# Kernel tuning notes

Measured on AMD Instinct MI355X. Metric: run time of the kernel, lower is better.

The kernel has to match this reference:

```python
import jax, jax.numpy as jnp
import numpy as np

B, S, H = 2, 1024, 2048          # batch, seq, hidden
E, K = 8, 2                       # num experts, top-k
I = 1408                          # moe_intermediate_size
IS = 5632                         # shared_expert_intermediate_size
WSCALE = 0.02


def setup_inputs() -> dict:
    key = jax.random.key(0)
    ks = jax.random.split(key, 9)
    f32 = jnp.float32
    return {
        "hidden_states": jax.random.normal(ks[0], (B, S, H), dtype=f32),
        "gate_w": jax.random.normal(ks[1], (E, H), dtype=f32) * WSCALE,          # router
        "w_gate": jax.random.normal(ks[2], (E, H, I), dtype=f32) * WSCALE,       # experts.N.gate_proj
        "w_up": jax.random.normal(ks[3], (E, H, I), dtype=f32) * WSCALE,         # experts.N.up_proj
        "w_down": jax.random.normal(ks[4], (E, I, H), dtype=f32) * WSCALE,       # experts.N.down_proj
        "sw_gate": jax.random.normal(ks[5], (H, IS), dtype=f32) * WSCALE,        # shared_expert.gate_proj
        "sw_up": jax.random.normal(ks[6], (H, IS), dtype=f32) * WSCALE,          # shared_expert.up_proj
        "sw_down": jax.random.normal(ks[7], (IS, H), dtype=f32) * WSCALE,        # shared_expert.down_proj
        "shared_gate_w": jax.random.normal(ks[8], (H, 1), dtype=f32) * WSCALE,   # shared_expert_gate
    }


def reference(hidden_states, gate_w, w_gate, w_up, w_down, sw_gate, sw_up, sw_down, shared_gate_w):
    x = hidden_states                                   # [B,S,H]
    # ---- TopKGate: softmax router -> top-k weights + indices, renormalized ----
    logits = jnp.einsum("bsh,eh->bse", x, gate_w)       # [B,S,E]
    probs = jax.nn.softmax(logits, axis=-1)
    top_w, top_i = jax.lax.top_k(probs, K)              # [B,S,K]
    top_w = top_w / jnp.sum(top_w, axis=-1, keepdims=True)
    # dense combine weights per expert: sum_k top_w * (top_i == e)  -> [B,S,E]
    onehot = jax.nn.one_hot(top_i, E, dtype=x.dtype)    # [B,S,K,E]
    combine = jnp.einsum("bsk,bske->bse", top_w, onehot)
    # ---- dense all-experts SwiGLU MLP, then mask/combine (faithful to source) ----
    g = jnp.einsum("bsh,ehi->besi", x, w_gate)          # [B,E,S,I]
    u = jnp.einsum("bsh,ehi->besi", x, w_up)
    h = jax.nn.silu(g) * u
    expert_out = jnp.einsum("besi,eih->besh", h, w_down)  # [B,E,S,H]
    moe_out = jnp.einsum("besh,bse->bsh", expert_out, combine)
    # ---- shared expert with sigmoid gate ----
    sh = jax.nn.silu(x @ sw_gate) * (x @ sw_up)         # [B,S,IS]
    shared_out = sh @ sw_down                            # [B,S,H]
    shared_gate = jax.nn.sigmoid(x @ shared_gate_w)     # [B,S,1]
    return moe_out + shared_out * shared_gate
```

## Files before the change

### kernel.cpp

```cpp
#include <hip/hip_runtime.h>
#include <hip/hip_bf16.h>
#include <stdint.h>

#define TOK   2048
#define HDIM  2048
#define IDIM  1408
#define ISDIM 5632
#define NEXP  8

typedef float  f32x4  __attribute__((ext_vector_type(4)));
typedef short  bf16x8 __attribute__((ext_vector_type(8)));

__device__ __forceinline__ unsigned short f2b(float f) {
  union { float f; uint32_t u; } v; v.f = f;
  return (unsigned short)((v.u + 0x7fffu + ((v.u >> 16) & 1u)) >> 16);
}

__global__ __launch_bounds__(256) void router_kernel(
    const float* __restrict__ X, const float* __restrict__ GW,
    const float* __restrict__ SGW, int* __restrict__ cnt,
    int* __restrict__ tok_e, float* __restrict__ tok_w, float* __restrict__ sg)
{
  const int tkn = blockIdx.x, t = threadIdx.x;
  const float* xr = X + (size_t)tkn * HDIM;
  float a[NEXP + 1];
  #pragma unroll
  for (int e = 0; e <= NEXP; ++e) a[e] = 0.f;
  for (int h = t; h < HDIM; h += 256) {
    const float xv = xr[h];
    #pragma unroll
    for (int e = 0; e < NEXP; ++e) a[e] += xv * GW[e * HDIM + h];
    a[NEXP] += xv * SGW[h];
  }
  #pragma unroll
  for (int off = 32; off > 0; off >>= 1) {
    #pragma unroll
    for (int e = 0; e <= NEXP; ++e) a[e] += __shfl_down(a[e], off);
  }
  __shared__ float red[4][NEXP + 1];
  if ((t & 63) == 0) {
    #pragma unroll
    for (int e = 0; e <= NEXP; ++e) red[t >> 6][e] = a[e];
  }
  __syncthreads();
  if (t == 0) {
    float l[NEXP + 1];
    #pragma unroll
    for (int e = 0; e <= NEXP; ++e) l[e] = red[0][e] + red[1][e] + red[2][e] + red[3][e];
    int i1 = 0;
    #pragma unroll
    for (int e = 1; e < NEXP; ++e) if (l[e] > l[i1]) i1 = e;
    int i2 = (i1 == 0) ? 1 : 0;
    #pragma unroll
    for (int e = 0; e < NEXP; ++e) if (e != i1 && e != i2 && l[e] > l[i2]) i2 = e;
    const float w1 = 1.f / (1.f + __expf(l[i2] - l[i1]));
    tok_e[tkn * 2 + 0] = i1; tok_e[tkn * 2 + 1] = i2;
    tok_w[tkn * 2 + 0] = w1; tok_w[tkn * 2 + 1] = 1.f - w1;
    atomicAdd(&cnt[i1], 1); atomicAdd(&cnt[i2], 1);
    sg[tkn] = 1.f / (1.f + __expf(-l[NEXP]));
  }
}

__global__ void scan_kernel(const int* __restrict__ cnt, int* __restrict__ offs) {
  if (threadIdx.x == 0) {
    int r = 0;
    for (int e = 0; e < NEXP; ++e) { offs[e] = r; r += cnt[e]; }
  }
}

__global__ __launch_bounds__(256) void build_kernel(
    const int* __restrict__ tok_e, const float* __restrict__ tok_w,
    const int* __restrict__ offs, int* __restrict__ cur,
    int* __restrict__ list, float* __restrict__ wl)
{
  const int tkn = blockIdx.x * 256 + threadIdx.x;
  if (tkn >= TOK) return;
  #pragma unroll
  for (int k = 0; k < 2; ++k) {
    const int e = tok_e[tkn * 2 + k];
    const int pos = atomicAdd(&cur[e], 1);
    const int slot = offs[e] + pos;
    list[slot] = tkn;
    wl[slot] = tok_w[tkn * 2 + k];
  }
}

__global__ __launch_bounds__(256) void cvt_kernel(
    const float* __restrict__ src, unsigned short* __restrict__ dst, int n4)
{
  const int i = blockIdx.x * 512 + threadIdx.x;
  #pragma unroll
  for (int p = 0; p < 2; ++p) {
    const int j = i + p * 256;
    if (j < n4) {
      const float4 v = ((const float4*)src)[j];
      ushort4 b; b.x = f2b(v.x); b.y = f2b(v.y); b.z = f2b(v.z); b.w = f2b(v.w);
      ((ushort4*)dst)[j] = b;
    }
  }
}

__global__ __launch_bounds__(256) void transpose_cvt_kernel(
    const float* __restrict__ src, unsigned short* __restrict__ dst,
    const int R, const int C)
{
  __shared__ unsigned short tile[64][72];
  const size_t mat = (size_t)blockIdx.z * R * C;
  const int c0 = blockIdx.x * 64, r0 = blockIdx.y * 64;
  const int t = threadIdx.x;
  const int rr = t >> 4, cc = (t & 15) * 4;
  #pragma unroll
  for (int p = 0; p < 4; ++p) {
    const int r = rr + p * 16;
    const float4 v = *(const float4*)(src + mat + (size_t)(r0 + r) * C + c0 + cc);
    tile[cc + 0][r] = f2b(v.x);
    tile[cc + 1][r] = f2b(v.y);
    tile[cc + 2][r] = f2b(v.z);
    tile[cc + 3][r] = f2b(v.w);
  }
  __syncthreads();
  #pragma unroll
  for (int p = 0; p < 2; ++p) {
    const int id = p * 256 + t;
    const int c = id >> 3, q = id & 7;
    const uint4 v = *(const uint4*)&tile[c][q * 8];
    *(uint4*)(dst + mat + (size_t)(c0 + c) * R + r0 + q * 8) = v;
  }
}


template<bool GATHER>
__global__ __launch_bounds__(256) void gateup_bf_kernel(
    const unsigned short* __restrict__ Xb,
    const unsigned short* __restrict__ WgT,
    const unsigned short* __restrict__ WuT,
    unsigned short* __restrict__ Cout,
    const int* __restrict__ list, const int* __restrict__ offs,
    const int* __restrict__ cnt, const int N)
{
  __shared__ char smem[49152];
  char* sA  = smem;
  char* sBg = smem + 16384;
  char* sBu = smem + 32768;

  const int t = threadIdx.x;
  const int nt = blockIdx.x;
  int rowbase, mcnt;
  const unsigned short *Wg, *Wu;
  if (GATHER) {
    const int e  = blockIdx.y >> 4;
    const int mt = blockIdx.y & 15;
    mcnt = cnt[e] - mt * 128;
    if (mcnt <= 0) return;
    rowbase = offs[e] + mt * 128;
    Wg = WgT + (size_t)e * N * HDIM;
    Wu = WuT + (size_t)e * N * HDIM;
  } else {
    rowbase = blockIdx.y * 128;
    mcnt = 128;
    Wg = WgT; Wu = WuT;
  }
  const int n0 = nt * 128;

  const int w = t >> 6, lane = t & 63;
  const int wr = w >> 1, wc = w & 1;
  const int lcol = lane & 15, lk = lane >> 4;

  f32x4 accg[4][4], accu[4][4];
  #pragma unroll
  for (int i = 0; i < 4; ++i)
    #pragma unroll
    for (int j = 0; j < 4; ++j) { accg[i][j] = {0.f,0.f,0.f,0.f}; accu[i][j] = {0.f,0.f,0.f,0.f}; }

  int arow[4], bm[4], koff[4];
  #pragma unroll
  for (int p = 0; p < 4; ++p) {
    const int s = p * 256 + t;
    const int m = s >> 3;
    bm[p] = m;
    koff[p] = ((s & 7) ^ (m & 7)) << 3;
    arow[p] = GATHER ? list[rowbase + m] : (rowbase + m);
  }

  const int KSTEPS = HDIM / 64;
  for (int kt = 0; kt < KSTEPS; ++kt) {
    const int k0 = kt * 64;
    if (kt) __syncthreads();
    #pragma unroll
    for (int p = 0; p < 4; ++p) {
      const int s16 = (p * 256 + t) * 16;
      *(uint4*)(sA  + s16) = *(const uint4*)(Xb + (size_t)arow[p] * HDIM + k0 + koff[p]);
      *(uint4*)(sBg + s16) = *(const uint4*)(Wg + (size_t)(n0 + bm[p]) * HDIM + k0 + koff[p]);
      *(uint4*)(sBu + s16) = *(const uint4*)(Wu + (size_t)(n0 + bm[p]) * HDIM + k0 + koff[p]);
    }
    __syncthreads();
    #pragma unroll
    for (int ks = 0; ks < 2; ++ks) {
      bf16x8 af[4], bg[4], bu[4];
      #pragma unroll
      for (int fm = 0; fm < 4; ++fm) {
        const int m = wr * 64 + fm * 16 + lcol;
        af[fm] = *(const bf16x8*)(sA + m * 128 + (((ks * 4 + lk) ^ (m & 7)) << 4));
      }
      #pragma unroll
      for (int fn = 0; fn < 4; ++fn) {
        const int n = wc * 64 + fn * 16 + lcol;
        const int ra = n * 128 + (((ks * 4 + lk) ^ (n & 7)) << 4);
        bg[fn] = *(const bf16x8*)(sBg + ra);
        bu[fn] = *(const bf16x8*)(sBu + ra);
      }
      #pragma unroll
      for (int fm = 0; fm < 4; ++fm)
        #pragma unroll
        for (int fn = 0; fn < 4; ++fn) {
          accg[fm][fn] = __builtin_amdgcn_mfma_f32_16x16x32_bf16(af[fm], bg[fn], accg[fm][fn], 0, 0, 0);
          accu[fm][fn] = __builtin_amdgcn_mfma_f32_16x16x32_bf16(af[fm], bu[fn], accu[fm][fn], 0, 0, 0);
        }
    }
  }
  #pragma unroll
  for (int fm = 0; fm < 4; ++fm) {
    #pragma unroll
    for (int fn = 0; fn < 4; ++fn) {
      const int col = n0 + wc * 64 + fn * 16 + lcol;
      #pragma unroll
      for (int r = 0; r < 4; ++r) {
        const int lrow = wr * 64 + fm * 16 + lk * 4 + r;
        if (lrow < mcnt) {
          const float gv = accg[fm][fn][r];
          const float uv = accu[fm][fn][r];
          const float hv = gv * uv / (1.f + __expf(-gv));
          Cout[(size_t)(rowbase + lrow) * N + col] = f2b(hv);
        }
      }
    }
  }
}

template<bool EXPERT>
__global__ __launch_bounds__(256) void down_bf_kernel(
    const unsigned short* __restrict__ Abuf,
    const unsigned short* __restrict__ BT,
    float* __restrict__ out,
    const int* __restrict__ list, const float* __restrict__ wl,
    const int* __restrict__ offs, const int* __restrict__ cnt, const int K)
{
  __shared__ char smem[32768];
  char* sA = smem;
  char* sB = smem + 16384;

  const int t = threadIdx.x;
  const int nt = blockIdx.x;
  int rowbase, mcnt;
  const unsigned short* Bm;
  if (EXPERT) {
    const int e  = blockIdx.y >> 4;
    const int mt = blockIdx.y & 15;
    mcnt = cnt[e] - mt * 128;
    if (mcnt <= 0) return;
    rowbase = offs[e] + mt * 128;
    Bm = BT + (size_t)e * HDIM * K;
  } else {
    rowbase = blockIdx.y * 128;
    mcnt = 128;
    Bm = BT;
  }
  const int n0 = nt * 128;
  const int w = t >> 6, lane = t & 63;
  const int wr = w >> 1, wc = w & 1;
  const int lcol = lane & 15, lk = lane >> 4;

  f32x4 acc[4][4];
  #pragma unroll
  for (int i = 0; i < 4; ++i)
    #pragma unroll
    for (int j = 0; j < 4; ++j) acc[i][j] = {0.f,0.f,0.f,0.f};

  int bm[4], koff[4];
  #pragma unroll
  for (int p = 0; p < 4; ++p) {
    const int s = p * 256 + t;
    const int m = s >> 3;
    bm[p] = m;
    koff[p] = ((s & 7) ^ (m & 7)) << 3;
  }

  const int KSTEPS = K / 64;
  for (int kt = 0; kt < KSTEPS; ++kt) {
    const int k0 = kt * 64;
    if (kt) __syncthreads();
    #pragma unroll
    for (int p = 0; p < 4; ++p) {
      const int s16 = (p * 256 + t) * 16;
      *(uint4*)(sA + s16) = *(const uint4*)(Abuf + (size_t)(rowbase + bm[p]) * K + k0 + koff[p]);
      *(uint4*)(sB + s16) = *(const uint4*)(Bm + (size_t)(n0 + bm[p]) * K + k0 + koff[p]);
    }
    __syncthreads();
    #pragma unroll
    for (int ks = 0; ks < 2; ++ks) {
      bf16x8 af[4], bfr[4];
      #pragma unroll
      for (int fm = 0; fm < 4; ++fm) {
        const int m = wr * 64 + fm * 16 + lcol;
        af[fm] = *(const bf16x8*)(sA + m * 128 + (((ks * 4 + lk) ^ (m & 7)) << 4));
      }
      #pragma unroll
      for (int fn = 0; fn < 4; ++fn) {
        const int n = wc * 64 + fn * 16 + lcol;
        bfr[fn] = *(const bf16x8*)(sB + n * 128 + (((ks * 4 + lk) ^ (n & 7)) << 4));
      }
      #pragma unroll
      for (int fm = 0; fm < 4; ++fm)
        #pragma unroll
        for (int fn = 0; fn < 4; ++fn)
          acc[fm][fn] = __builtin_amdgcn_mfma_f32_16x16x32_bf16(af[fm], bfr[fn], acc[fm][fn], 0, 0, 0);
    }
  }
  #pragma unroll
  for (int fm = 0; fm < 4; ++fm) {
    #pragma unroll
    for (int fn = 0; fn < 4; ++fn) {
      const int col = n0 + wc * 64 + fn * 16 + lcol;
      #pragma unroll
      for (int r = 0; r < 4; ++r) {
        const int lrow = wr * 64 + fm * 16 + lk * 4 + r;
        if (lrow < mcnt) {
          const float v = acc[fm][fn][r];
          if (EXPERT) {
            const int slot = rowbase + lrow;
            atomicAdd(out + (size_t)list[slot] * HDIM + col, wl[slot] * v);
          } else {
            const int row = rowbase + lrow;
            out[(size_t)row * HDIM + col] = wl[row] * v;
          }
        }
      }
    }
  }
}

template<bool GATHER>
__global__ __launch_bounds__(256) void gateup_kernel(
    const float* __restrict__ X,
    const float* __restrict__ WgA, const float* __restrict__ WuA,
    unsigned short* __restrict__ Cout,
    const int* __restrict__ list, const int* __restrict__ offs,
    const int* __restrict__ cnt, const int N)
{
  __shared__ char smem[49152];
  char* sA  = smem;
  char* sBg = smem + 16384;
  char* sBu = smem + 32768;
  const int t = threadIdx.x;
  const int nt = blockIdx.x;
  int rowbase, mcnt;
  const float *Wg, *Wu;
  if (GATHER) {
    const int e  = blockIdx.y >> 4;
    const int mt = blockIdx.y & 15;
    mcnt = cnt[e] - mt * 128;
    if (mcnt <= 0) return;
    rowbase = offs[e] + mt * 128;
    Wg = WgA + (size_t)e * HDIM * N;
    Wu = WuA + (size_t)e * HDIM * N;
  } else {
    rowbase = blockIdx.y * 128;
    mcnt = 128;
    Wg = WgA; Wu = WuA;
  }
  const int n0 = nt * 128;
  const int w = t >> 6, lane = t & 63;
  const int wr = w >> 1, wc = w & 1;
  const int lcol = lane & 15, lk = lane >> 4;
  f32x4 accg[4][4], accu[4][4];
  #pragma unroll
  for (int i = 0; i < 4; ++i)
    #pragma unroll
    for (int j = 0; j < 4; ++j) { accg[i][j] = {0.f,0.f,0.f,0.f}; accu[i][j] = {0.f,0.f,0.f,0.f}; }
  int arow[8];
  #pragma unroll
  for (int p = 0; p < 8; ++p) {
    const int m = p * 16 + (t >> 4);
    arow[p] = GATHER ? list[rowbase + m] : (rowbase + m);
  }
  const int ak4 = (t & 15) << 2;
  const int bn = t & 127, bkh = t >> 7;
  const int KSTEPS = HDIM / 64;
  for (int kt = 0; kt < KSTEPS; ++kt) {
    const int k0 = kt * 64;
    if (kt) __syncthreads();
    #pragma unroll
    for (int p = 0; p < 8; ++p) {
      const int m = p * 16 + (t >> 4);
      const float4 v = *(const float4*)(X + (size_t)arow[p] * HDIM + k0 + ak4);
      ushort4 b; b.x = f2b(v.x); b.y = f2b(v.y); b.z = f2b(v.z); b.w = f2b(v.w);
      *(ushort4*)(sA + m * 128 + ((((ak4 >> 3) ^ (m & 7)) << 4) | ((ak4 & 7) << 1))) = b;
    }
    #pragma unroll
    for (int p = 0; p < 8; ++p) {
      const int k4 = (p << 1) | bkh;
      const size_t gb = (size_t)(k0 + (k4 << 2)) * N + n0 + bn;
      const int wa = bn * 128 + ((((k4 >> 1) ^ (bn & 7)) << 4) | ((k4 & 1) << 3));
      ushort4 vg, vu;
      vg.x = f2b(Wg[gb]);                 vu.x = f2b(Wu[gb]);
      vg.y = f2b(Wg[gb + (size_t)N]);     vu.y = f2b(Wu[gb + (size_t)N]);
      vg.z = f2b(Wg[gb + 2*(size_t)N]);   vu.z = f2b(Wu[gb + 2*(size_t)N]);
      vg.w = f2b(Wg[gb + 3*(size_t)N]);   vu.w = f2b(Wu[gb + 3*(size_t)N]);
      *(ushort4*)(sBg + wa) = vg;
      *(ushort4*)(sBu + wa) = vu;
    }
    __syncthreads();
    #pragma unroll
    for (int ks = 0; ks < 2; ++ks) {
      bf16x8 af[4], bg[4], bu[4];
      #pragma unroll
      for (int fm = 0; fm < 4; ++fm) {
        const int m = wr * 64 + fm * 16 + lcol;
        af[fm] = *(const bf16x8*)(sA + m * 128 + (((ks * 4 + lk) ^ (m & 7)) << 4));
      }
      #pragma unroll
      for (int fn = 0; fn < 4; ++fn) {
        const int n = wc * 64 + fn * 16 + lcol;
        const int ra = n * 128 + (((ks * 4 + lk) ^ (n & 7)) << 4);
        bg[fn] = *(const bf16x8*)(sBg + ra);
        bu[fn] = *(const bf16x8*)(sBu + ra);
      }
      #pragma unroll
      for (int fm = 0; fm < 4; ++fm)
        #pragma unroll
        for (int fn = 0; fn < 4; ++fn) {
          accg[fm][fn] = __builtin_amdgcn_mfma_f32_16x16x32_bf16(af[fm], bg[fn], accg[fm][fn], 0, 0, 0);
          accu[fm][fn] = __builtin_amdgcn_mfma_f32_16x16x32_bf16(af[fm], bu[fn], accu[fm][fn], 0, 0, 0);
        }
    }
  }
  #pragma unroll
  for (int fm = 0; fm < 4; ++fm) {
    #pragma unroll
    for (int fn = 0; fn < 4; ++fn) {
      const int col = n0 + wc * 64 + fn * 16 + lcol;
      #pragma unroll
      for (int r = 0; r < 4; ++r) {
        const int lrow = wr * 64 + fm * 16 + lk * 4 + r;
        if (lrow < mcnt) {
          const float gv = accg[fm][fn][r];
          const float uv = accu[fm][fn][r];
          Cout[(size_t)(rowbase + lrow) * N + col] = f2b(gv * uv / (1.f + __expf(-gv)));
        }
      }
    }
  }
}

template<bool EXPERT>
__global__ __launch_bounds__(256) void down_kernel(
    const unsigned short* __restrict__ Abuf,
    const float* __restrict__ Ball,
    float* __restrict__ out,
    const int* __restrict__ list, const float* __restrict__ wl,
    const int* __restrict__ offs, const int* __restrict__ cnt, const int K)
{
  __shared__ char smem[32768];
  char* sA = smem;
  char* sB = smem + 16384;
  const int t = threadIdx.x;
  const int nt = blockIdx.x;
  int rowbase, mcnt;
  const float* Bm;
  if (EXPERT) {
    const int e  = blockIdx.y >> 4;
    const int mt = blockIdx.y & 15;
    mcnt = cnt[e] - mt * 128;
    if (mcnt <= 0) return;
    rowbase = offs[e] + mt * 128;
    Bm = Ball + (size_t)e * K * HDIM;
  } else {
    rowbase = blockIdx.y * 128;
    mcnt = 128;
    Bm = Ball;
  }
  const int n0 = nt * 128;
  const int w = t >> 6, lane = t & 63;
  const int wr = w >> 1, wc = w & 1;
  const int lcol = lane & 15, lk = lane >> 4;
  f32x4 acc[4][4];
  #pragma unroll
  for (int i = 0; i < 4; ++i)
    #pragma unroll
    for (int j = 0; j < 4; ++j) acc[i][j] = {0.f,0.f,0.f,0.f};
  const int bn = t & 127, bkh = t >> 7;
  const int KSTEPS = K / 64;
  for (int kt = 0; kt < KSTEPS; ++kt) {
    const int k0 = kt * 64;
    if (kt) __syncthreads();
    #pragma unroll
    for (int p = 0; p < 4; ++p) {
      const int s = p * 256 + t;
      const int m = s >> 3;
      const int k8 = (s & 7) ^ (m & 7);
      const uint4 v = *(const uint4*)(Abuf + (size_t)(rowbase + m) * K + k0 + (k8 << 3));
      *(uint4*)(sA + s * 16) = v;
    }
    #pragma unroll
    for (int p = 0; p < 8; ++p) {
      const int k4 = (p << 1) | bkh;
      const size_t gb = (size_t)(k0 + (k4 << 2)) * HDIM + n0 + bn;
      const int wa = bn * 128 + ((((k4 >> 1) ^ (bn & 7)) << 4) | ((k4 & 1) << 3));
      ushort4 vb;
      vb.x = f2b(Bm[gb]);
      vb.y = f2b(Bm[gb + HDIM]);
      vb.z = f2b(Bm[gb + 2 * HDIM]);
      vb.w = f2b(Bm[gb + 3 * HDIM]);
      *(ushort4*)(sB + wa) = vb;
    }
    __syncthreads();
    #pragma unroll
    for (int ks = 0; ks < 2; ++ks) {
      bf16x8 af[4], bfr[4];
      #pragma unroll
      for (int fm = 0; fm < 4; ++fm) {
        const int m = wr * 64 + fm * 16 + lcol;
        af[fm] = *(const bf16x8*)(sA + m * 128 + (((ks * 4 + lk) ^ (m & 7)) << 4));
      }
      #pragma unroll
      for (int fn = 0; fn < 4; ++fn) {
        const int n = wc * 64 + fn * 16 + lcol;
        bfr[fn] = *(const bf16x8*)(sB + n * 128 + (((ks * 4 + lk) ^ (n & 7)) << 4));
      }
      #pragma unroll
      for (int fm = 0; fm < 4; ++fm)
        #pragma unroll
        for (int fn = 0; fn < 4; ++fn)
          acc[fm][fn] = __builtin_amdgcn_mfma_f32_16x16x32_bf16(af[fm], bfr[fn], acc[fm][fn], 0, 0, 0);
    }
  }
  #pragma unroll
  for (int fm = 0; fm < 4; ++fm) {
    #pragma unroll
    for (int fn = 0; fn < 4; ++fn) {
      const int col = n0 + wc * 64 + fn * 16 + lcol;
      #pragma unroll
      for (int r = 0; r < 4; ++r) {
        const int lrow = wr * 64 + fm * 16 + lk * 4 + r;
        if (lrow < mcnt) {
          const float v = acc[fm][fn][r];
          if (EXPERT) {
            const int slot = rowbase + lrow;
            atomicAdd(out + (size_t)list[slot] * HDIM + col, wl[slot] * v);
          } else {
            const int row = rowbase + lrow;
            out[(size_t)row * HDIM + col] = wl[row] * v;
          }
        }
      }
    }
  }
}

extern "C" void kernel_launch(void* const* d_in, const int* in_sizes, int n_in,
                              void* d_out, int out_size, void* d_ws, size_t ws_size,
                              hipStream_t stream)
{
  const float* x       = (const float*)d_in[0];
  const float* gate_w  = (const float*)d_in[1];
  const float* w_gate  = (const float*)d_in[2];
  const float* w_up    = (const float*)d_in[3];
  const float* w_down  = (const float*)d_in[4];
  const float* sw_gate = (const float*)d_in[5];
  const float* sw_up   = (const float*)d_in[6];
  const float* sw_down = (const float*)d_in[7];
  const float* sgw     = (const float*)d_in[8];

  float* out = (float*)d_out;
  char* ws = (char*)d_ws;

  const size_t NEED = 136000000;

  if (ws_size >= NEED) {
    unsigned short* Xb   = (unsigned short*)ws;
    unsigned short* R1a  = (unsigned short*)(ws + 8388608);
    unsigned short* R1b  = (unsigned short*)(ws + 54525952);
    unsigned short* shb  = (unsigned short*)(ws + 100663296);
    unsigned short* hb   = (unsigned short*)(ws + 123731968);
    char* meta = ws + 135626752;
    int*   cnt   = (int*)(meta);
    int*   cur   = (int*)(meta + 256);
    int*   offs  = (int*)(meta + 512);
    int*   list  = (int*)(meta + 768);
    float* wl    = (float*)(meta + 768 + 17152);
    int*   tok_e = (int*)(meta + 768 + 2 * 17152);
    float* tok_w = (float*)(meta + 768 + 2 * 17152 + 16384);
    float* sg    = (float*)(meta + 768 + 2 * 17152 + 32768);

    hipMemsetAsync(meta, 0, 768 + 2 * 17152, stream);

    cvt_kernel<<<TOK * HDIM / 4 / 512, 256, 0, stream>>>(x, Xb, TOK * HDIM / 4);
    router_kernel<<<TOK, 256, 0, stream>>>(x, gate_w, sgw, cnt, tok_e, tok_w, sg);
    scan_kernel<<<1, 64, 0, stream>>>(cnt, offs);
    build_kernel<<<8, 256, 0, stream>>>(tok_e, tok_w, offs, cur, list, wl);

    transpose_cvt_kernel<<<dim3(ISDIM / 64, HDIM / 64, 1), 256, 0, stream>>>(sw_gate, R1a, HDIM, ISDIM);
    transpose_cvt_kernel<<<dim3(ISDIM / 64, HDIM / 64, 1), 256, 0, stream>>>(sw_up,   R1b, HDIM, ISDIM);
    gateup_bf_kernel<false><<<dim3(ISDIM / 128, TOK / 128), 256, 0, stream>>>(
        Xb, R1a, R1b, shb, nullptr, nullptr, nullptr, ISDIM);
    transpose_cvt_kernel<<<dim3(HDIM / 64, ISDIM / 64, 1), 256, 0, stream>>>(sw_down, R1a, ISDIM, HDIM);
    down_bf_kernel<false><<<dim3(HDIM / 128, TOK / 128), 256, 0, stream>>>(
        shb, R1a, out, nullptr, sg, nullptr, nullptr, ISDIM);
    transpose_cvt_kernel<<<dim3(IDIM / 64, HDIM / 64, NEXP), 256, 0, stream>>>(w_gate, R1a, HDIM, IDIM);
    transpose_cvt_kernel<<<dim3(IDIM / 64, HDIM / 64, NEXP), 256, 0, stream>>>(w_up,   R1b, HDIM, IDIM);
    gateup_bf_kernel<true><<<dim3(IDIM / 128, NEXP * 16), 256, 0, stream>>>(
        Xb, R1a, R1b, hb, list, offs, cnt, IDIM);
    transpose_cvt_kernel<<<dim3(HDIM / 64, IDIM / 64, NEXP), 256, 0, stream>>>(w_down, R1a, IDIM, HDIM);
    down_bf_kernel<true><<<dim3(HDIM / 128, NEXP * 16), 256, 0, stream>>>(
        hb, R1a, out, list, wl, offs, cnt, IDIM);
  } else {
    unsigned short* sh_buf = (unsigned short*)ws;
    unsigned short* h_buf  = (unsigned short*)(ws + 23068672);
    char* meta = ws + 34963456;
    int*   cnt   = (int*)(meta);
    int*   cur   = (int*)(meta + 256);
    int*   offs  = (int*)(meta + 512);
    int*   list  = (int*)(meta + 768);
    float* wl    = (float*)(meta + 768 + 17152);
    int*   tok_e = (int*)(meta + 768 + 2 * 17152);
    float* tok_w = (float*)(meta + 768 + 2 * 17152 + 16384);
    float* sg    = (float*)(meta + 768 + 2 * 17152 + 32768);

    hipMemsetAsync(meta, 0, 768 + 2 * 17152, stream);
    router_kernel<<<TOK, 256, 0, stream>>>(x, gate_w, sgw, cnt, tok_e, tok_w, sg);
    scan_kernel<<<1, 64, 0, stream>>>(cnt, offs);
    build_kernel<<<8, 256, 0, stream>>>(tok_e, tok_w, offs, cur, list, wl);
    gateup_kernel<false><<<dim3(ISDIM / 128, TOK / 128), 256, 0, stream>>>(
        x, sw_gate, sw_up, sh_buf, nullptr, nullptr, nullptr, ISDIM);
    down_kernel<false><<<dim3(HDIM / 128, TOK / 128), 256, 0, stream>>>(
        sh_buf, sw_down, out, nullptr, sg, nullptr, nullptr, ISDIM);
    gateup_kernel<true><<<dim3(IDIM / 128, NEXP * 16), 256, 0, stream>>>(
        x, w_gate, w_up, h_buf, list, offs, cnt, IDIM);
    down_kernel<true><<<dim3(HDIM / 128, NEXP * 16), 256, 0, stream>>>(
        h_buf, w_down, out, list, wl, offs, cnt, IDIM);
  }
}
```

Before: 645.4 us.

## Use direct global-to-LDS loads, XCD-aware block swizzle, and split-K shared down-proj

```diff
diff --git a/kernel.cpp b/kernel.cpp
--- a/kernel.cpp
+++ b/kernel.cpp
@@ -14,6 +14,12 @@
 __device__ __forceinline__ unsigned short f2b(float f) {
   union { float f; uint32_t u; } v; v.f = f;
   return (unsigned short)((v.u + 0x7fffu + ((v.u >> 16) & 1u)) >> 16);
+}
+
+__device__ __forceinline__ void async16(void* lds, const void* g) {
+  __builtin_amdgcn_global_load_lds(
+      (const __attribute__((address_space(1))) unsigned int*)g,
+      (__attribute__((address_space(3))) unsigned int*)lds, 16, 0, 0);
 }
 
 __global__ __launch_bounds__(256) void router_kernel(
@@ -136,31 +142,35 @@
     const unsigned short* __restrict__ WuT,
     unsigned short* __restrict__ Cout,
     const int* __restrict__ list, const int* __restrict__ offs,
-    const int* __restrict__ cnt, const int N)
+    const int* __restrict__ cnt, const int N, const int NT)
 {
   __shared__ char smem[49152];
   char* sA  = smem;
   char* sBg = smem + 16384;
   char* sBu = smem + 32768;
 
+  int wg = blockIdx.x;
+  wg = (wg & 7) * (gridDim.x >> 3) + (wg >> 3);
+  const int mt = wg & 15;
+  const int pn = wg >> 4;
+
   const int t = threadIdx.x;
-  const int nt = blockIdx.x;
-  int rowbase, mcnt;
+  int rowbase, mcnt, n0;
   const unsigned short *Wg, *Wu;
   if (GATHER) {
-    const int e  = blockIdx.y >> 4;
-    const int mt = blockIdx.y & 15;
+    const int e = pn / NT, n = pn % NT;
     mcnt = cnt[e] - mt * 128;
     if (mcnt <= 0) return;
     rowbase = offs[e] + mt * 128;
+    n0 = n * 128;
     Wg = WgT + (size_t)e * N * HDIM;
     Wu = WuT + (size_t)e * N * HDIM;
   } else {
-    rowbase = blockIdx.y * 128;
+    rowbase = mt * 128;
     mcnt = 128;
+    n0 = pn * 128;
     Wg = WgT; Wu = WuT;
   }
-  const int n0 = nt * 128;
 
   const int w = t >> 6, lane = t & 63;
   const int wr = w >> 1, wc = w & 1;
@@ -188,10 +198,10 @@
     if (kt) __syncthreads();
     #pragma unroll
     for (int p = 0; p < 4; ++p) {
-      const int s16 = (p * 256 + t) * 16;
-      *(uint4*)(sA  + s16) = *(const uint4*)(Xb + (size_t)arow[p] * HDIM + k0 + koff[p]);
-      *(uint4*)(sBg + s16) = *(const uint4*)(Wg + (size_t)(n0 + bm[p]) * HDIM + k0 + koff[p]);
-      *(uint4*)(sBu + s16) = *(const uint4*)(Wu + (size_t)(n0 + bm[p]) * HDIM + k0 + koff[p]);
+      const int lb = (p * 256 + (t & 192)) * 16;
+      async16(sA  + lb, Xb + (size_t)arow[p] * HDIM + k0 + koff[p]);
+      async16(sBg + lb, Wg + (size_t)(n0 + bm[p]) * HDIM + k0 + koff[p]);
+      async16(sBu + lb, Wu + (size_t)(n0 + bm[p]) * HDIM + k0 + koff[p]);
     }
     __syncthreads();
     #pragma unroll
@@ -237,35 +247,41 @@
   }
 }
 
-template<bool EXPERT>
+template<bool EXPERT, int KSPLIT>
 __global__ __launch_bounds__(256) void down_bf_kernel(
     const unsigned short* __restrict__ Abuf,
     const unsigned short* __restrict__ BT,
     float* __restrict__ out,
     const int* __restrict__ list, const float* __restrict__ wl,
-    const int* __restrict__ offs, const int* __restrict__ cnt, const int K)
+    const int* __restrict__ offs, const int* __restrict__ cnt,
+    const int K, const int ktps)
 {
   __shared__ char smem[32768];
   char* sA = smem;
   char* sB = smem + 16384;
 
+  int wg = blockIdx.x;
+  wg = (wg & 7) * (gridDim.x >> 3) + (wg >> 3);
+  const int ksp = wg % KSPLIT;
+  const int mt  = (wg / KSPLIT) & 15;
+  const int pn  = wg / (KSPLIT * 16);
+
   const int t = threadIdx.x;
-  const int nt = blockIdx.x;
-  int rowbase, mcnt;
+  int rowbase, mcnt, n0;
   const unsigned short* Bm;
   if (EXPERT) {
-    const int e  = blockIdx.y >> 4;
-    const int mt = blockIdx.y & 15;
+    const int e = pn >> 4, n = pn & 15;
     mcnt = cnt[e] - mt * 128;
     if (mcnt <= 0) return;
     rowbase = offs[e] + mt * 128;
+    n0 = n * 128;
     Bm = BT + (size_t)e * HDIM * K;
   } else {
-    rowbase = blockIdx.y * 128;
+    rowbase = mt * 128;
     mcnt = 128;
+    n0 = pn * 128;
     Bm = BT;
   }
-  const int n0 = nt * 128;
   const int w = t >> 6, lane = t & 63;
   const int wr = w >> 1, wc = w & 1;
   const int lcol = lane & 15, lk = lane >> 4;
@@ -285,15 +301,15 @@
     koff[p] = ((s & 7) ^ (m & 7)) << 3;
   }
 
-  const int KSTEPS = K / 64;
-  for (int kt = 0; kt < KSTEPS; ++kt) {
+  const int kbeg = ksp * ktps, kend = kbeg + ktps;
+  for (int kt = kbeg; kt < kend; ++kt) {
     const int k0 = kt * 64;
-    if (kt) __syncthreads();
+    if (kt != kbeg) __syncthreads();
     #pragma unroll
     for (int p = 0; p < 4; ++p) {
-      const int s16 = (p * 256 + t) * 16;
-      *(uint4*)(sA + s16) = *(const uint4*)(Abuf + (size_t)(rowbase + bm[p]) * K + k0 + koff[p]);
-      *(uint4*)(sB + s16) = *(const uint4*)(Bm + (size_t)(n0 + bm[p]) * K + k0 + koff[p]);
+      const int lb = (p * 256 + (t & 192)) * 16;
+      async16(sA + lb, Abuf + (size_t)(rowbase + bm[p]) * K + k0 + koff[p]);
+      async16(sB + lb, Bm + (size_t)(n0 + bm[p]) * K + k0 + koff[p]);
     }
     __syncthreads();
     #pragma unroll
@@ -331,7 +347,7 @@
             atomicAdd(out + (size_t)list[slot] * HDIM + col, wl[slot] * v);
           } else {
             const int row = rowbase + lrow;
-            out[(size_t)row * HDIM + col] = wl[row] * v;
+            atomicAdd(out + (size_t)row * HDIM + col, wl[row] * v);
           }
         }
       }
@@ -593,6 +609,7 @@
     float* sg    = (float*)(meta + 768 + 2 * 17152 + 32768);
 
     hipMemsetAsync(meta, 0, 768 + 2 * 17152, stream);
+    hipMemsetAsync(out, 0, (size_t)TOK * HDIM * 4, stream);
 
     cvt_kernel<<<TOK * HDIM / 4 / 512, 256, 0, stream>>>(x, Xb, TOK * HDIM / 4);
     router_kernel<<<TOK, 256, 0, stream>>>(x, gate_w, sgw, cnt, tok_e, tok_w, sg);
@@ -601,18 +618,18 @@
 
     transpose_cvt_kernel<<<dim3(ISDIM / 64, HDIM / 64, 1), 256, 0, stream>>>(sw_gate, R1a, HDIM, ISDIM);
     transpose_cvt_kernel<<<dim3(ISDIM / 64, HDIM / 64, 1), 256, 0, stream>>>(sw_up,   R1b, HDIM, ISDIM);
-    gateup_bf_kernel<false><<<dim3(ISDIM / 128, TOK / 128), 256, 0, stream>>>(
-        Xb, R1a, R1b, shb, nullptr, nullptr, nullptr, ISDIM);
+    gateup_bf_kernel<false><<<704, 256, 0, stream>>>(
+        Xb, R1a, R1b, shb, nullptr, nullptr, nullptr, ISDIM, 44);
     transpose_cvt_kernel<<<dim3(HDIM / 64, ISDIM / 64, 1), 256, 0, stream>>>(sw_down, R1a, ISDIM, HDIM);
-    down_bf_kernel<false><<<dim3(HDIM / 128, TOK / 128), 256, 0, stream>>>(
-        shb, R1a, out, nullptr, sg, nullptr, nullptr, ISDIM);
+    down_bf_kernel<false, 2><<<512, 256, 0, stream>>>(
+        shb, R1a, out, nullptr, sg, nullptr, nullptr, ISDIM, (ISDIM / 64) / 2);
     transpose_cvt_kernel<<<dim3(IDIM / 64, HDIM / 64, NEXP), 256, 0, stream>>>(w_gate, R1a, HDIM, IDIM);
     transpose_cvt_kernel<<<dim3(IDIM / 64, HDIM / 64, NEXP), 256, 0, stream>>>(w_up,   R1b, HDIM, IDIM);
-    gateup_bf_kernel<true><<<dim3(IDIM / 128, NEXP * 16), 256, 0, stream>>>(
-        Xb, R1a, R1b, hb, list, offs, cnt, IDIM);
+    gateup_bf_kernel<true><<<1408, 256, 0, stream>>>(
+        Xb, R1a, R1b, hb, list, offs, cnt, IDIM, 11);
     transpose_cvt_kernel<<<dim3(HDIM / 64, IDIM / 64, NEXP), 256, 0, stream>>>(w_down, R1a, IDIM, HDIM);
-    down_bf_kernel<true><<<dim3(HDIM / 128, NEXP * 16), 256, 0, stream>>>(
-        hb, R1a, out, list, wl, offs, cnt, IDIM);
+    down_bf_kernel<true, 1><<<2048, 256, 0, stream>>>(
+        hb, R1a, out, list, wl, offs, cnt, IDIM, IDIM / 64);
   } else {
     unsigned short* sh_buf = (unsigned short*)ws;
     unsigned short* h_buf  = (unsigned short*)(ws + 23068672);
```

New measurement: 674.9 us. +4.6%, slower.
